# Kernel optimization log

Measured on AMD Instinct MI355X. Metric: run time of the kernel, lower is better.

The kernel has to match this reference:

```python
import jax, jax.numpy as jnp
import numpy as np

COMMITMENT_COST = 0.25


def setup_inputs() -> dict:
    key = jax.random.key(0)
    k1, k2 = jax.random.split(key)
    B, S, D, K = 16, 4096, 256, 4096
    inputs = jax.random.normal(k1, (B, S, D), dtype=jnp.float32)
    # codebook ~ embedding.weight (init scale irrelevant for correctness baseline)
    codebook = jax.random.normal(k2, (K, D), dtype=jnp.float32)
    return {"inputs": inputs, "codebook": codebook}


def reference(inputs, codebook):
    B, S, D = inputs.shape
    flat = inputs.reshape(-1, D)  # (N, D)
    distances = (
        jnp.sum(flat * flat, axis=1, keepdims=True)
        + jnp.sum(codebook * codebook, axis=1)
        - 2.0 * jnp.matmul(flat, codebook.T)
    )
    encoding_indices = jnp.argmin(distances, axis=1)  # (N,)
    quantized = codebook[encoding_indices].reshape(inputs.shape)  # gather
    # commitment loss: beta * mse(inputs, sg(quantized))
    diff = inputs - jax.lax.stop_gradient(quantized)
    commitment_loss = COMMITMENT_COST * jnp.mean(diff * diff)
    # straight-through estimator
    quantized_st = inputs + jax.lax.stop_gradient(quantized - inputs)
    return quantized_st, commitment_loss, encoding_indices
```

## Files before the change

kernel.cpp:

```cpp
#include <hip/hip_runtime.h>
#include <stdint.h>

typedef _Float16 half8 __attribute__((ext_vector_type(8)));
typedef float f32x4 __attribute__((ext_vector_type(4)));

#define DDIM 256
#define KCODES 4096
#define BM 128
#define BN 256
#define NCH 8
#define STEPS 128
#define DELTA 0.02f
#define FLT_BIG 3.4e38f

#define GLOAD_LDS(gsrc, ldst)                                                        \
    __builtin_amdgcn_global_load_lds(                                                \
        (const __attribute__((address_space(1))) void*)(const void*)(gsrc),          \
        (__attribute__((address_space(3))) void*)(void*)(ldst), 16, 0, 0)

__global__ void cvt_hl_kernel(const float* __restrict__ src, half8* __restrict__ dst) {
    int gid = blockIdx.x * 256 + threadIdx.x;
    int p = gid & 7;
    int ch = (gid >> 3) & 7;
    long row = gid >> 6;
    int part = p >> 2, quad = p & 3;
    const float* s = src + row * DDIM + ch * 32 + quad * 8;
    half8 h;
    #pragma unroll
    for (int j = 0; j < 8; ++j) {
        float v = s[j];
        _Float16 hi = (_Float16)v;
        h[j] = part ? (_Float16)(v - (float)hi) : hi;
    }
    dst[gid] = h;
}

__global__ void enorm_kernel(const float* __restrict__ cb, float* __restrict__ en, int K) {
    int gid = blockIdx.x * blockDim.x + threadIdx.x;
    int code = gid >> 6;
    int lane = threadIdx.x & 63;
    if (code >= K) return;
    const float4 v = *reinterpret_cast<const float4*>(&cb[(size_t)code * DDIM + lane * 4]);
    float s = v.x * v.x + v.y * v.y + v.z * v.z + v.w * v.w;
    #pragma unroll
    for (int off = 32; off > 0; off >>= 1) s += __shfl_xor(s, off, 64);
    if (lane == 0) en[code] = s;
}

__global__ __launch_bounds__(512, 2)
void vq_mfma_kernel(const half8* x16, const half8* __restrict__ cb16,
                    const float* __restrict__ en, const float* __restrict__ x,
                    const float* __restrict__ cb, float* out,
                    int* __restrict__ list, int* __restrict__ counter,
                    float* __restrict__ loss_accum, int N) {
    __shared__ __align__(16) half8 Abuf[2][BM * 8];
    __shared__ __align__(16) half8 Bbuf[2][BN * 8];
    __shared__ float en_lds[KCODES];
    __shared__ float red_d[4][BM];
    __shared__ float red_d2[4][BM];
    __shared__ int   red_i[4][BM];
    __shared__ int   binfo[BM];
    __shared__ float wsum[8];

    const int tid = threadIdx.x;
    const int lane = tid & 63;
    const int w = tid >> 6;
    const int wr = w >> 2, wc = w & 3;
    const int l15 = lane & 15, l4 = lane >> 4;
    const int brow = blockIdx.x * BM;
    const size_t ND = (size_t)N * DDIM;

    ((float4*)en_lds)[tid] = ((const float4*)en)[tid];
    ((float4*)en_lds)[tid + 512] = ((const float4*)en)[tid + 512];

    const int lrow = lane >> 3;
    const int swz = (lane & 7) ^ lrow;
    const half8* pA0 = x16 + ((size_t)(brow + w * 8       + lrow) * NCH) * 8 + swz;
    const half8* pA1 = x16 + ((size_t)(brow + (w + 8) * 8 + lrow) * NCH) * 8 + swz;
    const half8* pB0 = cb16 + ((size_t)((w     ) * 8 + lrow) * NCH) * 8 + swz;
    const half8* pB1 = cb16 + ((size_t)((w +  8) * 8 + lrow) * NCH) * 8 + swz;
    const half8* pB2 = cb16 + ((size_t)((w + 16) * 8 + lrow) * NCH) * 8 + swz;
    const half8* pB3 = cb16 + ((size_t)((w + 24) * 8 + lrow) * NCH) * 8 + swz;

#define STAGE(b_) do {                                      \
        GLOAD_LDS(pA0, &Abuf[b_][(w     ) * 64]);           \
        GLOAD_LDS(pA1, &Abuf[b_][(w +  8) * 64]);           \
        GLOAD_LDS(pB0, &Bbuf[b_][(w     ) * 64]);           \
        GLOAD_LDS(pB1, &Bbuf[b_][(w +  8) * 64]);           \
        GLOAD_LDS(pB2, &Bbuf[b_][(w + 16) * 64]);           \
        GLOAD_LDS(pB3, &Bbuf[b_][(w + 24) * 64]);           \
    } while (0)

#define ADVANCE(t_) do {                                    \
        int dA = (((t_) & 7) == 7) ? -56 : 8;               \
        int dB = (((t_) & 7) == 7) ? 16328 : 8;             \
        pA0 += dA; pA1 += dA;                               \
        pB0 += dB; pB1 += dB; pB2 += dB; pB3 += dB;         \
    } while (0)

    const int sw7 = l15 & 7;
    const _Float16* A0 = (const _Float16*)Abuf;
    const _Float16* B0 = (const _Float16*)Bbuf;
    const _Float16* aH = A0 + wr * 4096 + l15 * 64 + ((l4    ) ^ sw7) * 8;
    const _Float16* aL = A0 + wr * 4096 + l15 * 64 + ((l4 + 4) ^ sw7) * 8;
    const _Float16* bH = B0 + wc * 4096 + l15 * 64 + ((l4    ) ^ sw7) * 8;
    const _Float16* bL = B0 + wc * 4096 + l15 * 64 + ((l4 + 4) ^ sw7) * 8;

    STAGE(0); ADVANCE(0);
    STAGE(1); ADVANCE(1);
    __syncthreads();

    half8 Pah[4], Pal[4], Pbh[4], Pbl[4];
    half8 Qah[4], Qal[4], Qbh[4], Qbl[4];

#define LOADF(T, AO, BO) do {                                         \
        _Pragma("unroll") for (int i_ = 0; i_ < 4; ++i_) {            \
            T##ah[i_] = *(const half8*)(aH + (AO) + i_ * 1024);       \
            T##al[i_] = *(const half8*)(aL + (AO) + i_ * 1024);       \
            T##bh[i_] = *(const half8*)(bH + (BO) + i_ * 1024);       \
            T##bl[i_] = *(const half8*)(bL + (BO) + i_ * 1024);       \
        }                                                             \
    } while (0)

#define MFMA48(T) do {                                                \
        _Pragma("unroll") for (int m_ = 0; m_ < 4; ++m_)              \
        _Pragma("unroll") for (int n_ = 0; n_ < 4; ++n_) {            \
            acc[m_][n_] = __builtin_amdgcn_mfma_f32_16x16x32_f16(T##bh[m_], T##ah[n_], acc[m_][n_], 0, 0, 0); \
            acc[m_][n_] = __builtin_amdgcn_mfma_f32_16x16x32_f16(T##bl[m_], T##ah[n_], acc[m_][n_], 0, 0, 0); \
            acc[m_][n_] = __builtin_amdgcn_mfma_f32_16x16x32_f16(T##bh[m_], T##al[n_], acc[m_][n_], 0, 0, 0); \
        }                                                             \
    } while (0)

    f32x4 acc[4][4];
    float bestv[4], best2v[4];
    int bidv[4];
    #pragma unroll
    for (int i = 0; i < 4; ++i) { bestv[i] = FLT_BIG; best2v[i] = FLT_BIG; bidv[i] = 0; }

    LOADF(P, 0, 0);
    asm volatile("s_waitcnt lgkmcnt(0)" ::: "memory");
    __builtin_amdgcn_sched_barrier(0);

    const int code_sub = wc * 64 + l4 * 4;

    for (int s = 0; s < STEPS; s += 2) {
        if ((s & 7) == 0) {
            #pragma unroll
            for (int m = 0; m < 4; ++m)
                #pragma unroll
                for (int n = 0; n < 4; ++n) acc[m][n] = (f32x4){0.f, 0.f, 0.f, 0.f};
        }
        if (s + 2 < STEPS) { STAGE(0); ADVANCE(s + 2); }
        LOADF(Q, 8192, 16384);
        __builtin_amdgcn_s_setprio(1);
        MFMA48(P);
        __builtin_amdgcn_s_setprio(0);
        __syncthreads();

        if (s + 3 < STEPS) { STAGE(1); ADVANCE(s + 3); }
        if (s + 2 < STEPS) LOADF(P, 0, 0);
        __builtin_amdgcn_s_setprio(1);
        MFMA48(Q);
        __builtin_amdgcn_s_setprio(0);
        if ((s & 7) == 6) {
            const int c0 = ((s + 1) >> 3) * BN;
            #pragma unroll
            for (int m = 0; m < 4; ++m) {
                #pragma unroll
                for (int r = 0; r < 4; ++r) {
                    int code = c0 + code_sub + m * 16 + r;
                    float e = en_lds[code];
                    #pragma unroll
                    for (int n = 0; n < 4; ++n) {
                        float dist = fmaf(-2.f, acc[m][n][r], e);
                        if (dist < bestv[n]) { best2v[n] = bestv[n]; bestv[n] = dist; bidv[n] = code; }
                        else if (dist < best2v[n]) best2v[n] = dist;
                    }
                }
            }
        }
        __syncthreads();
    }
#undef STAGE
#undef ADVANCE
#undef LOADF
#undef MFMA48

    #pragma unroll
    for (int n = 0; n < 4; ++n) {
        float d = bestv[n], d2 = best2v[n];
        int ix = bidv[n];
        #pragma unroll
        for (int off = 16; off < 64; off <<= 1) {
            float od = __shfl_xor(d, off, 64);
            float od2 = __shfl_xor(d2, off, 64);
            int oi = __shfl_xor(ix, off, 64);
            if (od < d || (od == d && oi < ix)) { d2 = fminf(d, od2); d = od; ix = oi; }
            else d2 = fminf(d2, od);
        }
        if (l4 == 0) {
            int row = wr * 64 + n * 16 + l15;
            red_d[wc][row] = d;
            red_d2[wc][row] = d2;
            red_i[wc][row] = ix;
        }
    }
    __syncthreads();

    if (tid < BM) {
        float d = red_d[0][tid], d2 = red_d2[0][tid];
        int ix = red_i[0][tid];
        #pragma unroll
        for (int q = 1; q < 4; ++q) {
            float od = red_d[q][tid], od2 = red_d2[q][tid];
            int oi = red_i[q][tid];
            if (od < d || (od == d && oi < ix)) { d2 = fminf(d, od2); d = od; ix = oi; }
            else d2 = fminf(d2, od);
        }
        int fl = (d2 - d < DELTA) ? 1 : 0;
        out[ND + 1 + brow + tid] = (float)ix;
        binfo[tid] = ix | (fl << 16);
        if (fl) {
            int pos = atomicAdd(counter, 1);
            list[pos] = brow + tid;
        }
    }
    __syncthreads();

    float lsum = 0.f;
    #pragma unroll 4
    for (int pp = 0; pp < 16; ++pp) {
        int i = tid + pp * 512;
        int row = i >> 6;
        int c4 = (i & 63) << 2;
        int info = binfo[row];
        int code = info & 0xffff;
        const float4 q = *reinterpret_cast<const float4*>(&cb[(size_t)code * DDIM + c4]);
        const float4 xv = *reinterpret_cast<const float4*>(&x[(size_t)(brow + row) * DDIM + c4]);
        float d0 = xv.x - q.x, d1 = xv.y - q.y, d2 = xv.z - q.z, d3 = xv.w - q.w;
        if (!(info >> 16)) lsum += d0 * d0 + d1 * d1 + d2 * d2 + d3 * d3;
        *reinterpret_cast<float4*>(&out[(size_t)(brow + row) * DDIM + c4]) = q;
    }
    #pragma unroll
    for (int off = 32; off > 0; off >>= 1) lsum += __shfl_xor(lsum, off, 64);
    if (lane == 0) wsum[w] = lsum;
    __syncthreads();
    if (tid == 0) {
        float tot = 0.f;
        #pragma unroll
        for (int q = 0; q < 8; ++q) tot += wsum[q];
        atomicAdd(loss_accum, tot * (0.25f / (float)ND));
    }
}

__global__ __launch_bounds__(256)
void rescan_kernel(const float* __restrict__ x, const float* __restrict__ cb,
                   const float* __restrict__ en, const int* __restrict__ list,
                   const int* __restrict__ counter, float* out,
                   float* __restrict__ loss_accum, int N) {
    __shared__ __align__(16) float4 xrow4[64];
    __shared__ float wd[4];
    __shared__ int wi[4];
    __shared__ float wls[4];
    __shared__ int six;
    const int tid = threadIdx.x;
    const int w = tid >> 6;
    const int lane = tid & 63;
    const int cnt = *counter;
    const size_t ND = (size_t)N * DDIM;

    for (int it = blockIdx.x; it < cnt; it += gridDim.x) {
        const int row = list[it];
        __syncthreads();
        if (tid < 64) xrow4[tid] = ((const float4*)&x[(size_t)row * DDIM])[tid];
        __syncthreads();
        const float4 xv = xrow4[lane];
        float bd = FLT_BIG;
        int bi = 0;
        for (int i = 0; i < KCODES / 4; ++i) {
            int code = i * 4 + w;
            const float4 c4 = ((const float4*)&cb[(size_t)code * DDIM])[lane];
            float s = xv.x * c4.x + xv.y * c4.y + xv.z * c4.z + xv.w * c4.w;
            #pragma unroll
            for (int off = 1; off < 64; off <<= 1) s += __shfl_xor(s, off, 64);
            float dist = fmaf(-2.f, s, en[code]);
            if (dist < bd) { bd = dist; bi = code; }
        }
        if (lane == 0) { wd[w] = bd; wi[w] = bi; }
        __syncthreads();
        if (tid == 0) {
            float d = wd[0]; int ix = wi[0];
            #pragma unroll
            for (int q = 1; q < 4; ++q) {
                if (wd[q] < d || (wd[q] == d && wi[q] < ix)) { d = wd[q]; ix = wi[q]; }
            }
            six = ix;
            out[ND + 1 + row] = (float)ix;
        }
        __syncthreads();
        const int ix = six;
        float c = cb[(size_t)ix * DDIM + tid];
        float xs = ((const float*)xrow4)[tid];
        out[(size_t)row * DDIM + tid] = c;
        float dd = xs - c;
        float ss = dd * dd;
        #pragma unroll
        for (int off = 32; off > 0; off >>= 1) ss += __shfl_xor(ss, off, 64);
        if (lane == 0) wls[w] = ss;
        __syncthreads();
        if (tid == 0) {
            float tot = wls[0] + wls[1] + wls[2] + wls[3];
            atomicAdd(loss_accum, tot * (0.25f / (float)ND));
        }
    }
}

__global__ void loss_fin_kernel(const float* __restrict__ loss_accum,
                                float* __restrict__ out, size_t off) {
    if (blockIdx.x == 0 && threadIdx.x == 0) out[off] = *loss_accum;
}

extern "C" void kernel_launch(void* const* d_in, const int* in_sizes, int n_in,
                              void* d_out, int out_size, void* d_ws, size_t ws_size,
                              hipStream_t stream) {
    const float* x = (const float*)d_in[0];
    const float* cb = (const float*)d_in[1];
    const int N = in_sizes[0] / DDIM;
    const int K = in_sizes[1] / DDIM;
    float* out = (float*)d_out;

    half8* x16 = (half8*)d_out;

    half8* cb16 = (half8*)d_ws;
    char* p = (char*)d_ws + (4 << 20);
    float* en = (float*)p;                  p += (size_t)K * 4;
    int* list = (int*)p;                    p += (size_t)N * 4;
    int* counter = (int*)p;                 p += 64;
    float* loss_accum = (float*)p;

    hipMemsetAsync(counter, 0, sizeof(int), stream);
    hipMemsetAsync(loss_accum, 0, sizeof(float), stream);
    cvt_hl_kernel<<<(N * 64) / 256, 256, 0, stream>>>(x, x16);
    cvt_hl_kernel<<<(K * 64) / 256, 256, 0, stream>>>(cb, cb16);
    enorm_kernel<<<(K * 64) / 256, 256, 0, stream>>>(cb, en, K);
    vq_mfma_kernel<<<N / BM, 512, 0, stream>>>(x16, cb16, en, x, cb, out,
                                               list, counter, loss_accum, N);
    rescan_kernel<<<512, 256, 0, stream>>>(x, cb, en, list, counter, out, loss_accum, N);
    loss_fin_kernel<<<1, 64, 0, stream>>>(loss_accum, out, (size_t)N * DDIM);
}
```

Before: 732.0 us.

## Restructure GEMM main loop to one sync per k-step with fully unrolled inner loop

Replaces the two-stage register double-buffered loop (P/Q fragment sets, two barriers per pair of steps) with an outer loop over 16 code tiles and a fully unrolled 8-step inner loop. Each step has a single barrier, issues the next global->LDS stage, then loads fragments and runs MFMAs. The aim is to cut barrier count and register pressure and to let the compiler schedule more freely with constant offsets. In exchange it drops register-level prefetch of the next fragments, so LDS read latency may be exposed before the MFMAs.

```diff
diff --git a/kernel.cpp b/kernel.cpp
--- a/kernel.cpp
+++ b/kernel.cpp
@@ -91,9 +91,9 @@
         GLOAD_LDS(pB3, &Bbuf[b_][(w + 24) * 64]);           \
     } while (0)
 
-#define ADVANCE(t_) do {                                    \
-        int dA = (((t_) & 7) == 7) ? -56 : 8;               \
-        int dB = (((t_) & 7) == 7) ? 16328 : 8;             \
+#define ADVANCE(roll_) do {                                 \
+        const int dA = (roll_) ? -56 : 8;                   \
+        const int dB = (roll_) ? 16328 : 8;                 \
         pA0 += dA; pA1 += dA;                               \
         pB0 += dB; pB1 += dB; pB2 += dB; pB3 += dB;         \
     } while (0)
@@ -106,85 +106,74 @@
     const _Float16* bH = B0 + wc * 4096 + l15 * 64 + ((l4    ) ^ sw7) * 8;
     const _Float16* bL = B0 + wc * 4096 + l15 * 64 + ((l4 + 4) ^ sw7) * 8;
 
-    STAGE(0); ADVANCE(0);
-    STAGE(1); ADVANCE(1);
-    __syncthreads();
-
-    half8 Pah[4], Pal[4], Pbh[4], Pbl[4];
-    half8 Qah[4], Qal[4], Qbh[4], Qbl[4];
-
-#define LOADF(T, AO, BO) do {                                         \
-        _Pragma("unroll") for (int i_ = 0; i_ < 4; ++i_) {            \
-            T##ah[i_] = *(const half8*)(aH + (AO) + i_ * 1024);       \
-            T##al[i_] = *(const half8*)(aL + (AO) + i_ * 1024);       \
-            T##bh[i_] = *(const half8*)(bH + (BO) + i_ * 1024);       \
-            T##bl[i_] = *(const half8*)(bL + (BO) + i_ * 1024);       \
-        }                                                             \
-    } while (0)
-
-#define MFMA48(T) do {                                                \
-        _Pragma("unroll") for (int m_ = 0; m_ < 4; ++m_)              \
-        _Pragma("unroll") for (int n_ = 0; n_ < 4; ++n_) {            \
-            acc[m_][n_] = __builtin_amdgcn_mfma_f32_16x16x32_f16(T##bh[m_], T##ah[n_], acc[m_][n_], 0, 0, 0); \
-            acc[m_][n_] = __builtin_amdgcn_mfma_f32_16x16x32_f16(T##bl[m_], T##ah[n_], acc[m_][n_], 0, 0, 0); \
-            acc[m_][n_] = __builtin_amdgcn_mfma_f32_16x16x32_f16(T##bh[m_], T##al[n_], acc[m_][n_], 0, 0, 0); \
-        }                                                             \
-    } while (0)
-
-    f32x4 acc[4][4];
+    STAGE(0); ADVANCE(0 );
+
     float bestv[4], best2v[4];
     int bidv[4];
     #pragma unroll
     for (int i = 0; i < 4; ++i) { bestv[i] = FLT_BIG; best2v[i] = FLT_BIG; bidv[i] = 0; }
 
-    LOADF(P, 0, 0);
-    asm volatile("s_waitcnt lgkmcnt(0)" ::: "memory");
-    __builtin_amdgcn_sched_barrier(0);
-
     const int code_sub = wc * 64 + l4 * 4;
-
-    for (int s = 0; s < STEPS; s += 2) {
-        if ((s & 7) == 0) {
+    f32x4 acc[4][4];
+
+    for (int it = 0; it < 16; ++it) {
+        #pragma unroll
+        for (int m = 0; m < 4; ++m)
+            #pragma unroll
+            for (int n = 0; n < 4; ++n) acc[m][n] = (f32x4){0.f, 0.f, 0.f, 0.f};
+
+        #pragma unroll
+        for (int k = 0; k < 8; ++k) {
+            __syncthreads();
+            if (k != 7) {
+                STAGE((k + 1) & 1);
+                ADVANCE(k == 6);
+            } else if (it != 15) {
+                STAGE(0);
+                ADVANCE(0);
+            }
+            __builtin_amdgcn_sched_barrier(0);
+
+            const int ao = (k & 1) ? 8192 : 0;
+            const int bo = (k & 1) ? 16384 : 0;
+            half8 ah[4], al[4], bh[4], bl[4];
+            #pragma unroll
+            for (int i = 0; i < 4; ++i) {
+                ah[i] = *(const half8*)(aH + ao + i * 1024);
+                al[i] = *(const half8*)(aL + ao + i * 1024);
+                bh[i] = *(const half8*)(bH + bo + i * 1024);
+                bl[i] = *(const half8*)(bL + bo + i * 1024);
+            }
+            __builtin_amdgcn_s_setprio(1);
             #pragma unroll
             for (int m = 0; m < 4; ++m)
                 #pragma unroll
-                for (int n = 0; n < 4; ++n) acc[m][n] = (f32x4){0.f, 0.f, 0.f, 0.f};
-        }
-        if (s + 2 < STEPS) { STAGE(0); ADVANCE(s + 2); }
-        LOADF(Q, 8192, 16384);
-        __builtin_amdgcn_s_setprio(1);
-        MFMA48(P);
-        __builtin_amdgcn_s_setprio(0);
-        __syncthreads();
-
-        if (s + 3 < STEPS) { STAGE(1); ADVANCE(s + 3); }
-        if (s + 2 < STEPS) LOADF(P, 0, 0);
-        __builtin_amdgcn_s_setprio(1);
-        MFMA48(Q);
-        __builtin_amdgcn_s_setprio(0);
-        if ((s & 7) == 6) {
-            const int c0 = ((s + 1) >> 3) * BN;
-            #pragma unroll
-            for (int m = 0; m < 4; ++m) {
+                for (int n = 0; n < 4; ++n) {
+                    acc[m][n] = __builtin_amdgcn_mfma_f32_16x16x32_f16(bh[m], ah[n], acc[m][n], 0, 0, 0);
+                    acc[m][n] = __builtin_amdgcn_mfma_f32_16x16x32_f16(bl[m], ah[n], acc[m][n], 0, 0, 0);
+                    acc[m][n] = __builtin_amdgcn_mfma_f32_16x16x32_f16(bh[m], al[n], acc[m][n], 0, 0, 0);
+                }
+            __builtin_amdgcn_s_setprio(0);
+        }
+
+        const int c0 = it * BN;
+        #pragma unroll
+        for (int m = 0; m < 4; ++m) {
+            #pragma unroll
+            for (int r = 0; r < 4; ++r) {
+                int code = c0 + code_sub + m * 16 + r;
+                float e = en_lds[code];
                 #pragma unroll
-                for (int r = 0; r < 4; ++r) {
-                    int code = c0 + code_sub + m * 16 + r;
-                    float e = en_lds[code];
-                    #pragma unroll
-                    for (int n = 0; n < 4; ++n) {
-                        float dist = fmaf(-2.f, acc[m][n][r], e);
-                        if (dist < bestv[n]) { best2v[n] = bestv[n]; bestv[n] = dist; bidv[n] = code; }
-                        else if (dist < best2v[n]) best2v[n] = dist;
-                    }
+                for (int n = 0; n < 4; ++n) {
+                    float dist = fmaf(-2.f, acc[m][n][r], e);
+                    if (dist < bestv[n]) { best2v[n] = bestv[n]; bestv[n] = dist; bidv[n] = code; }
+                    else if (dist < best2v[n]) best2v[n] = dist;
                 }
             }
         }
-        __syncthreads();
     }
 #undef STAGE
 #undef ADVANCE
-#undef LOADF
-#undef MFMA48
 
     #pragma unroll
     for (int n = 0; n < 4; ++n) {
```

After: 710.6 us. -2.9%, faster.
